# Kernel tuning notes

Measured on AMD Instinct MI355X. Metric: run time of the kernel, lower is better.

The kernel has to match this reference:

```python
import jax, jax.numpy as jnp
import numpy as np

N, E, D, L = 50000, 800000, 64, 3
EPS = 1e-5


def setup_inputs() -> dict:
    key = jax.random.key(0)
    ks = jax.random.split(key, 12)
    x = jax.random.normal(ks[0], (N, D), dtype=jnp.float32)
    edge_index = jax.random.randint(ks[1], (2, E), 0, N, dtype=jnp.int64)
    w = lambda k: jax.random.normal(k, (L, D, D), dtype=jnp.float32) * 0.1
    return {
        "x": x,
        "edge_index": edge_index,
        "Wq": w(ks[2]), "bq": jnp.zeros((L, D), jnp.float32),
        "Wk": w(ks[3]), "bk": jnp.zeros((L, D), jnp.float32),
        "Wv": w(ks[4]), "bv": jnp.zeros((L, D), jnp.float32),
        "Ws": w(ks[5]), "bs": jnp.zeros((L, D), jnp.float32),
        "gamma": jnp.ones((L - 1, D), jnp.float32),
        "beta": jnp.zeros((L - 1, D), jnp.float32),
    }


def _transformer_conv(x, src, dst, Wq, bq, Wk, bk, Wv, bv, Ws, bs):
    # PyG TransformerConv, heads=1, concat=True, root_weight=True, beta=False
    n = x.shape[0]
    d = x.shape[1]
    q = x @ Wq + bq          # [N, D] query of target nodes
    k = x @ Wk + bk          # [N, D] key of source nodes
    v = x @ Wv + bv          # [N, D] value of source nodes
    skip = x @ Ws + bs       # root/skip term on target nodes
    scale = 1.0 / jnp.sqrt(jnp.asarray(d, x.dtype))
    s = jnp.sum(q[dst] * k[src], axis=-1) * scale        # [E] edge scores
    # segment softmax over incoming edges of each destination node
    m = jax.ops.segment_max(s, dst, num_segments=n)       # [N]
    e = jnp.exp(s - m[dst])                               # [E]
    denom = jax.ops.segment_sum(e, dst, num_segments=n)   # [N]
    alpha = e / denom[dst]                                # [E]
    agg = jax.ops.segment_sum(alpha[:, None] * v[src], dst, num_segments=n)  # [N, D]
    return agg + skip


def _batch_norm(x, gamma, beta):
    # nn.BatchNorm1d training-mode forward: batch stats over node dim, biased var
    mean = jnp.mean(x, axis=0)
    var = jnp.mean((x - mean) ** 2, axis=0)
    return gamma * (x - mean) * jax.lax.rsqrt(var + EPS) + beta


def reference(x, edge_index, Wq, bq, Wk, bk, Wv, bv, Ws, bs, gamma, beta):
    src, dst = edge_index[0], edge_index[1]
    num_layers = Wq.shape[0]
    h = x
    for l in range(num_layers):
        h = _transformer_conv(h, src, dst, Wq[l], bq[l], Wk[l], bk[l],
                              Wv[l], bv[l], Ws[l], bs[l])
        if l != num_layers - 1:
            h = _batch_norm(h, gamma[l], beta[l])
            h = jax.nn.relu(h)
    return h
```

## Files before the change

kernel.cpp:

```cpp
#include <hip/hip_runtime.h>
#include <math.h>

#define N_NODES 50000
#define N_EDGES 800000
#define EPSV 1e-5f
#define PROJ_NT 16
#define SCAN_NB ((N_NODES + 255) / 256)

__device__ __forceinline__ unsigned short f2bf(float f) {
    unsigned u = __float_as_uint(f);
    unsigned r = (u + 0x7fffu + ((u >> 16) & 1u)) >> 16;
    return (unsigned short)r;
}
__device__ __forceinline__ float bflo(unsigned u) { return __uint_as_float(u << 16); }
__device__ __forceinline__ float bfhi(unsigned u) { return __uint_as_float(u & 0xffff0000u); }


__global__ __launch_bounds__(256) void count_kernel(const int* __restrict__ dst,
                                                    int* __restrict__ cnt) {
    int e = blockIdx.x * 256 + threadIdx.x;
    if (e < N_EDGES) atomicAdd(&cnt[dst[e]], 1);
}

__global__ __launch_bounds__(256) void scan_blocksum(const int* __restrict__ cnt,
                                                     int* __restrict__ bsum) {
    __shared__ int red[256];
    int t = threadIdx.x;
    int i = blockIdx.x * 256 + t;
    red[t] = (i < N_NODES) ? cnt[i] : 0;
    __syncthreads();
#pragma unroll
    for (int o = 128; o > 0; o >>= 1) {
        if (t < o) red[t] += red[t + o];
        __syncthreads();
    }
    if (t == 0) bsum[blockIdx.x] = red[0];
}

__global__ __launch_bounds__(256) void scan_bsum(int* __restrict__ bsum) {
    __shared__ int buf[256];
    int t = threadIdx.x;
    int v = (t < SCAN_NB) ? bsum[t] : 0;
    buf[t] = v;
    __syncthreads();
#pragma unroll
    for (int o = 1; o < 256; o <<= 1) {
        int tv = (t >= o) ? buf[t - o] : 0;
        __syncthreads();
        buf[t] += tv;
        __syncthreads();
    }
    if (t < SCAN_NB) bsum[t] = buf[t] - v;
}

__global__ __launch_bounds__(256) void scan_final(int* __restrict__ cnt_cursor,
                                                  const int* __restrict__ bsum,
                                                  int* __restrict__ row_off) {
    __shared__ int buf[256];
    int t = threadIdx.x;
    int i = blockIdx.x * 256 + t;
    int v = (i < N_NODES) ? cnt_cursor[i] : 0;
    buf[t] = v;
    __syncthreads();
#pragma unroll
    for (int o = 1; o < 256; o <<= 1) {
        int tv = (t >= o) ? buf[t - o] : 0;
        __syncthreads();
        buf[t] += tv;
        __syncthreads();
    }
    int excl = buf[t] - v + bsum[blockIdx.x];
    if (i < N_NODES) {
        row_off[i]    = excl;
        cnt_cursor[i] = excl;
    }
    if (i == N_NODES) row_off[N_NODES] = N_EDGES;
}

__global__ __launch_bounds__(256) void scatter_kernel(const int* __restrict__ src,
                                                      const int* __restrict__ dst,
                                                      int* __restrict__ cursor,
                                                      unsigned short* __restrict__ ssrc) {
    int e = blockIdx.x * 256 + threadIdx.x;
    if (e < N_EDGES) {
        int d = dst[e];
        int p = atomicAdd(&cursor[d], 1);
        ssrc[p] = (unsigned short)src[e];
    }
}

__global__ __launch_bounds__(256) void fill_dst_kernel(const int* __restrict__ row_off,
                                                       unsigned short* __restrict__ sdst) {
    int n = blockIdx.x * 256 + threadIdx.x;
    if (n >= N_NODES) return;
    int b = row_off[n], e2 = row_off[n + 1];
    for (int p = b; p < e2; ++p) sdst[p] = (unsigned short)n;
}

template<bool BN>
__global__ __launch_bounds__(256) void proj_kernel(
    const float* __restrict__ hin,
    const float* __restrict__ Wq, const float* __restrict__ Wk,
    const float* __restrict__ Wv, const float* __restrict__ Ws,
    const float* __restrict__ bq, const float* __restrict__ bk,
    const float* __restrict__ bv, const float* __restrict__ bs,
    const float* __restrict__ bnp, const float* __restrict__ gamma,
    const float* __restrict__ beta,
    float* __restrict__ qb, unsigned short* __restrict__ kb,
    unsigned short* __restrict__ vb, float* __restrict__ skb)
{
    __shared__ float xs[16][64];
    const int t = threadIdx.x;
    const int m = t >> 6, c = t & 63;
    const float* Wm = (m == 0) ? Wq : (m == 1) ? Wk : (m == 2) ? Wv : Ws;
    const float* bm = (m == 0) ? bq : (m == 1) ? bk : (m == 2) ? bv : bs;
    float*          obase_f = ((m == 0) ? qb : skb) + c;
    unsigned short* obase_h = ((m == 1) ? kb : vb) + c;

    float w[64];
#pragma unroll
    for (int i = 0; i < 64; i++) w[i] = Wm[i * 64 + c];
    const float bias = bm[c];

    const int jj = t >> 4, i0 = (t & 15) * 4;
    float4 mu4, rs4, ga4, be4;
    if (BN) {
        mu4 = *(const float4*)&bnp[i0];
        rs4 = *(const float4*)&bnp[64 + i0];
        ga4 = *(const float4*)&gamma[i0];
        be4 = *(const float4*)&beta[i0];
    }

    const int nbase = blockIdx.x * PROJ_NT;
    for (int tile = 0; tile < PROJ_NT / 16; ++tile) {
        const int n0 = nbase + tile * 16;
        __syncthreads();
        {
            int node = n0 + jj;
            float4 xv = make_float4(0.f, 0.f, 0.f, 0.f);
            if (node < N_NODES) xv = *(const float4*)&hin[node * 64 + i0];
            if (BN) {
                xv.x = fmaxf(fmaf(ga4.x * (xv.x - mu4.x), rs4.x, be4.x), 0.f);
                xv.y = fmaxf(fmaf(ga4.y * (xv.y - mu4.y), rs4.y, be4.y), 0.f);
                xv.z = fmaxf(fmaf(ga4.z * (xv.z - mu4.z), rs4.z, be4.z), 0.f);
                xv.w = fmaxf(fmaf(ga4.w * (xv.w - mu4.w), rs4.w, be4.w), 0.f);
            }
            *(float4*)&xs[jj][i0] = xv;
        }
        __syncthreads();
#pragma unroll 4
        for (int j = 0; j < 16; j++) {
            const int node = n0 + j;
            if (node >= N_NODES) break;
            float a0 = bias, a1 = 0.f, a2 = 0.f, a3 = 0.f;
#pragma unroll
            for (int i4 = 0; i4 < 16; i4++) {
                float4 xv = *(const float4*)&xs[j][i4 * 4];
                a0 = fmaf(xv.x, w[i4 * 4 + 0], a0);
                a1 = fmaf(xv.y, w[i4 * 4 + 1], a1);
                a2 = fmaf(xv.z, w[i4 * 4 + 2], a2);
                a3 = fmaf(xv.w, w[i4 * 4 + 3], a3);
            }
            float r = (a0 + a1) + (a2 + a3);
            if (m == 0 || m == 3) obase_f[(size_t)node * 64] = r;
            else                  obase_h[(size_t)node * 64] = f2bf(r);
        }
    }
}

__global__ __launch_bounds__(256) void edge_kernel(const float* __restrict__ qb,
                                                   const unsigned short* __restrict__ kb,
                                                   const unsigned short* __restrict__ ssrc,
                                                   const unsigned short* __restrict__ sdst,
                                                   float* __restrict__ s_out) {
    int idx = blockIdx.x * 256 + threadIdx.x;
    int e   = idx >> 3;
    int l8  = idx & 7;
    if (e >= N_EDGES) return;
    int s = ssrc[e], d = sdst[e];
    const float4* qp = (const float4*)&qb[(size_t)d * 64 + l8 * 8];
    float4 q0 = qp[0], q1 = qp[1];
    uint4 kw = *(const uint4*)&kb[(size_t)s * 64 + l8 * 8];
    float acc = q0.x * bflo(kw.x) + q0.y * bfhi(kw.x)
              + q0.z * bflo(kw.y) + q0.w * bfhi(kw.y)
              + q1.x * bflo(kw.z) + q1.y * bfhi(kw.z)
              + q1.z * bflo(kw.w) + q1.w * bfhi(kw.w);
    acc += __shfl_xor(acc, 1);
    acc += __shfl_xor(acc, 2);
    acc += __shfl_xor(acc, 4);
    if (l8 == 0) s_out[e] = acc * 0.125f;
}

__global__ __launch_bounds__(256) void agg_kernel(const float* __restrict__ s_arr,
                                                  const unsigned short* __restrict__ vb,
                                                  const unsigned short* __restrict__ ssrc,
                                                  const int* __restrict__ row_off,
                                                  const float* __restrict__ skb,
                                                  float* __restrict__ out) {
    int tid  = blockIdx.x * 256 + threadIdx.x;
    int lane = threadIdx.x & 63;
    int l32  = lane & 31;
    int n    = (tid >> 6) * 2 + (lane >> 5);
    int beg = row_off[n], end = row_off[n + 1];
    float2 skv = ((const float2*)skb)[(size_t)n * 32 + l32];

    float mx = -INFINITY;
    for (int p = beg + l32; p < end; p += 32) mx = fmaxf(mx, s_arr[p]);
#pragma unroll
    for (int o = 16; o >= 1; o >>= 1) mx = fmaxf(mx, __shfl_xor(mx, o));

    const unsigned int* vw = (const unsigned int*)vb;
    const int sbase = lane & 32;
    float lsum = 0.f, accx = 0.f, accy = 0.f;
    int base = beg;
    while (true) {
        int cnt = end - base;
        cnt = cnt < 0 ? 0 : (cnt > 32 ? 32 : cnt);
        int cntm = max(cnt, __shfl_xor(cnt, 32));
        if (cntm == 0) break;
        float my_e = 0.f;
        int   my_s = 0;
        if (l32 < cnt) {
            my_e = __expf(s_arr[base + l32] - mx);
            my_s = (int)ssrc[base + l32];
        }
        lsum += my_e;
#pragma unroll 4
        for (int j = 0; j < cntm; ++j) {
            float w  = __shfl(my_e, sbase + j);
            int   sv = __shfl(my_s, sbase + j);
            unsigned vvw = vw[(size_t)sv * 32 + l32];
            accx = fmaf(w, bflo(vvw), accx);
            accy = fmaf(w, bfhi(vvw), accy);
        }
        base += 32;
    }
#pragma unroll
    for (int o = 16; o >= 1; o >>= 1) lsum += __shfl_xor(lsum, o);
    float inv = (end > beg) ? 1.f / lsum : 0.f;
    float2 r;
    r.x = fmaf(accx, inv, skv.x);
    r.y = fmaf(accy, inv, skv.y);
    ((float2*)out)[(size_t)n * 32 + l32] = r;
}

__global__ __launch_bounds__(256) void bn_stats_kernel(const float* __restrict__ h,
                                                       float* __restrict__ sums) {
    __shared__ float red[256], red2[256];
    int t = threadIdx.x;
    int d = t & 63, part = t >> 6;
    float s = 0.f, s2 = 0.f;
    for (int r = blockIdx.x * 4 + part; r < N_NODES; r += gridDim.x * 4) {
        float v = h[r * 64 + d];
        s += v;
        s2 = fmaf(v, v, s2);
    }
    red[t] = s; red2[t] = s2;
    __syncthreads();
    if (t < 64) {
        s  = red[t] + red[t + 64] + red[t + 128] + red[t + 192];
        s2 = red2[t] + red2[t + 64] + red2[t + 128] + red2[t + 192];
        atomicAdd(&sums[t], s);
        atomicAdd(&sums[64 + t], s2);
    }
}

__global__ void bn_final_kernel(const float* __restrict__ sums, float* __restrict__ bnp) {
    int d = threadIdx.x;
    if (d < 64) {
        float mean = sums[d] * (1.0f / N_NODES);
        float var  = sums[64 + d] * (1.0f / N_NODES) - mean * mean;
        bnp[d]      = mean;
        bnp[64 + d] = rsqrtf(var + EPSV);
    }
}


extern "C" void kernel_launch(void* const* d_in, const int* in_sizes, int n_in,
                              void* d_out, int out_size, void* d_ws, size_t ws_size,
                              hipStream_t stream) {
    const float* x     = (const float*)d_in[0];
    const int*   ei    = (const int*)d_in[1];
    const float* Wq    = (const float*)d_in[2];
    const float* bq    = (const float*)d_in[3];
    const float* Wk    = (const float*)d_in[4];
    const float* bk    = (const float*)d_in[5];
    const float* Wv    = (const float*)d_in[6];
    const float* bv    = (const float*)d_in[7];
    const float* Ws    = (const float*)d_in[8];
    const float* bs    = (const float*)d_in[9];
    const float* gamma = (const float*)d_in[10];
    const float* beta  = (const float*)d_in[11];
    float* out = (float*)d_out;

    char* wsp = (char*)d_ws;
    size_t off = 0;
    auto alloc = [&](size_t bytes) -> void* {
        void* p = wsp + off;
        off += (bytes + 255) / 256 * 256;
        return p;
    };
    float*          qb      = (float*)alloc((size_t)N_NODES * 64 * 4);
    unsigned short* kb      = (unsigned short*)alloc((size_t)N_NODES * 64 * 2);
    unsigned short* vb      = (unsigned short*)alloc((size_t)N_NODES * 64 * 2);
    float*          skb     = (float*)alloc((size_t)N_NODES * 64 * 4);
    float*          hbuf    = (float*)alloc((size_t)N_NODES * 64 * 4);
    float*          s_arr   = (float*)alloc((size_t)N_EDGES * 4);
    int*            row_off = (int*)alloc((size_t)(N_NODES + 1) * 4);
    int*            cursor  = (int*)alloc((size_t)N_NODES * 4);
    unsigned short* ssrc    = (unsigned short*)alloc((size_t)N_EDGES * 2);
    unsigned short* sdst    = (unsigned short*)alloc((size_t)N_EDGES * 2);
    int*            bsum    = (int*)alloc((size_t)SCAN_NB * 4);
    float*          sums    = (float*)alloc(128 * 4);
    float*          bnp     = (float*)alloc(128 * 4);

    const int* src = ei;
    const int* dst = ei + N_EDGES;

    hipMemsetAsync(cursor, 0, N_NODES * 4, stream);
    count_kernel<<<(N_EDGES + 255) / 256, 256, 0, stream>>>(dst, cursor);
    scan_blocksum<<<SCAN_NB, 256, 0, stream>>>(cursor, bsum);
    scan_bsum<<<1, 256, 0, stream>>>(bsum);
    scan_final<<<SCAN_NB, 256, 0, stream>>>(cursor, bsum, row_off);
    scatter_kernel<<<(N_EDGES + 255) / 256, 256, 0, stream>>>(src, dst, cursor, ssrc);
    fill_dst_kernel<<<SCAN_NB, 256, 0, stream>>>(row_off, sdst);

    const int proj_grid = (N_NODES + PROJ_NT - 1) / PROJ_NT;
    const int edge_grid = (N_EDGES * 8 + 255) / 256;
    const int agg_grid  = N_NODES / 8;

    for (int l = 0; l < 3; l++) {
        const float* hin = (l == 0) ? x : hbuf;
        if (l == 0) {
            proj_kernel<false><<<proj_grid, 256, 0, stream>>>(
                hin, Wq, Wk, Wv, Ws, bq, bk, bv, bs,
                bnp, gamma, beta, qb, kb, vb, skb);
        } else {
            proj_kernel<true><<<proj_grid, 256, 0, stream>>>(
                hin, Wq + l * 4096, Wk + l * 4096, Wv + l * 4096, Ws + l * 4096,
                bq + l * 64, bk + l * 64, bv + l * 64, bs + l * 64,
                bnp, gamma + (l - 1) * 64, beta + (l - 1) * 64, qb, kb, vb, skb);
        }
        edge_kernel<<<edge_grid, 256, 0, stream>>>(qb, kb, ssrc, sdst, s_arr);
        float* o = (l == 2) ? out : hbuf;
        agg_kernel<<<agg_grid, 256, 0, stream>>>(s_arr, vb, ssrc, row_off, skb, o);
        if (l < 2) {
            hipMemsetAsync(sums, 0, 128 * 4, stream);
            bn_stats_kernel<<<256, 256, 0, stream>>>(hbuf, sums);
            bn_final_kernel<<<1, 64, 0, stream>>>(sums, bnp);
        }
    }
}
```

Baseline: 401.5 us.

## Assign 8 lanes per node in aggregation and drop BN atomics and memset

The aggregation kernel now gives each destination node an 8-lane group with 16-byte bf16 value loads, instead of a 32-lane half-wavefront with 4-byte loads. This packs 8 nodes per wavefront and cuts idle lanes on low-degree nodes (average degree 16). The cost is a per-chunk max reduction across all groups in the wave, so every group loops to the wave's longest row. Separately, BN statistics now write per-block partials that a 128-thread final kernel reduces, which removes the atomics and the memset launch.

```diff
diff --git a/kernel.cpp b/kernel.cpp
--- a/kernel.cpp
+++ b/kernel.cpp
@@ -199,53 +199,74 @@
                                                   float* __restrict__ out) {
     int tid  = blockIdx.x * 256 + threadIdx.x;
     int lane = threadIdx.x & 63;
-    int l32  = lane & 31;
-    int n    = (tid >> 6) * 2 + (lane >> 5);
-    int beg = row_off[n], end = row_off[n + 1];
-    float2 skv = ((const float2*)skb)[(size_t)n * 32 + l32];
+    int l8   = lane & 7;
+    int g    = (tid >> 6) * 8 + (lane >> 3);
+    bool valid = g < N_NODES;
+    int beg = 0, end = 0;
+    float4 sk0 = make_float4(0, 0, 0, 0), sk1 = sk0;
+    if (valid) {
+        beg = row_off[g];
+        end = row_off[g + 1];
+        const float4* skp = (const float4*)&skb[(size_t)g * 64 + l8 * 8];
+        sk0 = skp[0];
+        sk1 = skp[1];
+    }
 
     float mx = -INFINITY;
-    for (int p = beg + l32; p < end; p += 32) mx = fmaxf(mx, s_arr[p]);
-#pragma unroll
-    for (int o = 16; o >= 1; o >>= 1) mx = fmaxf(mx, __shfl_xor(mx, o));
-
-    const unsigned int* vw = (const unsigned int*)vb;
-    const int sbase = lane & 32;
-    float lsum = 0.f, accx = 0.f, accy = 0.f;
+    for (int p = beg + l8; p < end; p += 8) mx = fmaxf(mx, s_arr[p]);
+    mx = fmaxf(mx, __shfl_xor(mx, 1));
+    mx = fmaxf(mx, __shfl_xor(mx, 2));
+    mx = fmaxf(mx, __shfl_xor(mx, 4));
+
+    const uint4* vw = (const uint4*)vb;
+    const int sbase = lane & 56;
+    float lsum = 0.f;
+    float a0 = 0, a1 = 0, a2 = 0, a3 = 0, a4 = 0, a5 = 0, a6 = 0, a7 = 0;
     int base = beg;
     while (true) {
         int cnt = end - base;
-        cnt = cnt < 0 ? 0 : (cnt > 32 ? 32 : cnt);
-        int cntm = max(cnt, __shfl_xor(cnt, 32));
+        cnt = cnt < 0 ? 0 : (cnt > 8 ? 8 : cnt);
+        int c = max(cnt, __shfl_xor(cnt, 8));
+        c = max(c, __shfl_xor(c, 16));
+        int cntm = max(c, __shfl_xor(c, 32));
         if (cntm == 0) break;
         float my_e = 0.f;
         int   my_s = 0;
-        if (l32 < cnt) {
-            my_e = __expf(s_arr[base + l32] - mx);
-            my_s = (int)ssrc[base + l32];
+        if (l8 < cnt) {
+            my_e = __expf(s_arr[base + l8] - mx);
+            my_s = (int)ssrc[base + l8];
         }
         lsum += my_e;
-#pragma unroll 4
+#pragma unroll 2
         for (int j = 0; j < cntm; ++j) {
             float w  = __shfl(my_e, sbase + j);
             int   sv = __shfl(my_s, sbase + j);
-            unsigned vvw = vw[(size_t)sv * 32 + l32];
-            accx = fmaf(w, bflo(vvw), accx);
-            accy = fmaf(w, bfhi(vvw), accy);
-        }
-        base += 32;
-    }
-#pragma unroll
-    for (int o = 16; o >= 1; o >>= 1) lsum += __shfl_xor(lsum, o);
-    float inv = (end > beg) ? 1.f / lsum : 0.f;
-    float2 r;
-    r.x = fmaf(accx, inv, skv.x);
-    r.y = fmaf(accy, inv, skv.y);
-    ((float2*)out)[(size_t)n * 32 + l32] = r;
+            uint4 vv = vw[(size_t)sv * 8 + l8];
+            a0 = fmaf(w, bflo(vv.x), a0); a1 = fmaf(w, bfhi(vv.x), a1);
+            a2 = fmaf(w, bflo(vv.y), a2); a3 = fmaf(w, bfhi(vv.y), a3);
+            a4 = fmaf(w, bflo(vv.z), a4); a5 = fmaf(w, bfhi(vv.z), a5);
+            a6 = fmaf(w, bflo(vv.w), a6); a7 = fmaf(w, bfhi(vv.w), a7);
+        }
+        base += 8;
+    }
+    lsum += __shfl_xor(lsum, 1);
+    lsum += __shfl_xor(lsum, 2);
+    lsum += __shfl_xor(lsum, 4);
+    if (valid) {
+        float inv = (end > beg) ? 1.f / lsum : 0.f;
+        float4 r0, r1;
+        r0.x = fmaf(a0, inv, sk0.x); r0.y = fmaf(a1, inv, sk0.y);
+        r0.z = fmaf(a2, inv, sk0.z); r0.w = fmaf(a3, inv, sk0.w);
+        r1.x = fmaf(a4, inv, sk1.x); r1.y = fmaf(a5, inv, sk1.y);
+        r1.z = fmaf(a6, inv, sk1.z); r1.w = fmaf(a7, inv, sk1.w);
+        float4* op = (float4*)&out[(size_t)g * 64 + l8 * 8];
+        op[0] = r0;
+        op[1] = r1;
+    }
 }
 
 __global__ __launch_bounds__(256) void bn_stats_kernel(const float* __restrict__ h,
-                                                       float* __restrict__ sums) {
+                                                       float* __restrict__ partials) {
     __shared__ float red[256], red2[256];
     int t = threadIdx.x;
     int d = t & 63, part = t >> 6;
@@ -260,18 +281,24 @@
     if (t < 64) {
         s  = red[t] + red[t + 64] + red[t + 128] + red[t + 192];
         s2 = red2[t] + red2[t + 64] + red2[t + 128] + red2[t + 192];
-        atomicAdd(&sums[t], s);
-        atomicAdd(&sums[64 + t], s2);
-    }
-}
-
-__global__ void bn_final_kernel(const float* __restrict__ sums, float* __restrict__ bnp) {
-    int d = threadIdx.x;
-    if (d < 64) {
-        float mean = sums[d] * (1.0f / N_NODES);
-        float var  = sums[64 + d] * (1.0f / N_NODES) - mean * mean;
-        bnp[d]      = mean;
-        bnp[64 + d] = rsqrtf(var + EPSV);
+        partials[blockIdx.x * 128 + t]      = s;
+        partials[blockIdx.x * 128 + 64 + t] = s2;
+    }
+}
+
+__global__ void bn_final_kernel(const float* __restrict__ partials,
+                                float* __restrict__ bnp) {
+    __shared__ float sh[128];
+    int t = threadIdx.x;
+    float a = 0.f;
+    for (int b = 0; b < 256; ++b) a += partials[b * 128 + t];
+    sh[t] = a;
+    __syncthreads();
+    if (t < 64) {
+        float mean = sh[t] * (1.0f / N_NODES);
+        float var  = sh[64 + t] * (1.0f / N_NODES) - mean * mean;
+        bnp[t]      = mean;
+        bnp[64 + t] = rsqrtf(var + EPSV);
     }
 }
 
@@ -300,19 +327,19 @@
         off += (bytes + 255) / 256 * 256;
         return p;
     };
-    float*          qb      = (float*)alloc((size_t)N_NODES * 64 * 4);
-    unsigned short* kb      = (unsigned short*)alloc((size_t)N_NODES * 64 * 2);
-    unsigned short* vb      = (unsigned short*)alloc((size_t)N_NODES * 64 * 2);
-    float*          skb     = (float*)alloc((size_t)N_NODES * 64 * 4);
-    float*          hbuf    = (float*)alloc((size_t)N_NODES * 64 * 4);
-    float*          s_arr   = (float*)alloc((size_t)N_EDGES * 4);
-    int*            row_off = (int*)alloc((size_t)(N_NODES + 1) * 4);
-    int*            cursor  = (int*)alloc((size_t)N_NODES * 4);
-    unsigned short* ssrc    = (unsigned short*)alloc((size_t)N_EDGES * 2);
-    unsigned short* sdst    = (unsigned short*)alloc((size_t)N_EDGES * 2);
-    int*            bsum    = (int*)alloc((size_t)SCAN_NB * 4);
-    float*          sums    = (float*)alloc(128 * 4);
-    float*          bnp     = (float*)alloc(128 * 4);
+    float*          qb       = (float*)alloc((size_t)N_NODES * 64 * 4);
+    unsigned short* kb       = (unsigned short*)alloc((size_t)N_NODES * 64 * 2);
+    unsigned short* vb       = (unsigned short*)alloc((size_t)N_NODES * 64 * 2);
+    float*          skb      = (float*)alloc((size_t)N_NODES * 64 * 4);
+    float*          hbuf     = (float*)alloc((size_t)N_NODES * 64 * 4);
+    float*          s_arr    = (float*)alloc((size_t)N_EDGES * 4);
+    int*            row_off  = (int*)alloc((size_t)(N_NODES + 1) * 4);
+    int*            cursor   = (int*)alloc((size_t)N_NODES * 4);
+    unsigned short* ssrc     = (unsigned short*)alloc((size_t)N_EDGES * 2);
+    unsigned short* sdst     = (unsigned short*)alloc((size_t)N_EDGES * 2);
+    int*            bsum     = (int*)alloc((size_t)SCAN_NB * 4);
+    float*          partials = (float*)alloc(256 * 128 * 4);
+    float*          bnp      = (float*)alloc(128 * 4);
 
     const int* src = ei;
     const int* dst = ei + N_EDGES;
@@ -327,7 +354,7 @@
 
     const int proj_grid = (N_NODES + PROJ_NT - 1) / PROJ_NT;
     const int edge_grid = (N_EDGES * 8 + 255) / 256;
-    const int agg_grid  = N_NODES / 8;
+    const int agg_grid  = (N_NODES + 31) / 32;
 
     for (int l = 0; l < 3; l++) {
         const float* hin = (l == 0) ? x : hbuf;
@@ -345,9 +372,8 @@
         float* o = (l == 2) ? out : hbuf;
         agg_kernel<<<agg_grid, 256, 0, stream>>>(s_arr, vb, ssrc, row_off, skb, o);
         if (l < 2) {
-            hipMemsetAsync(sums, 0, 128 * 4, stream);
-            bn_stats_kernel<<<256, 256, 0, stream>>>(hbuf, sums);
-            bn_final_kernel<<<1, 64, 0, stream>>>(sums, bnp);
-        }
-    }
-}
+            bn_stats_kernel<<<256, 256, 0, stream>>>(hbuf, partials);
+            bn_final_kernel<<<1, 128, 0, stream>>>(partials, bnp);
+        }
+    }
+}
```

Measured after the change: 358.3 us (median of 2 runs). -10.7%, faster.
